# Optimization experiments

Measured on AMD Instinct MI355X. Metric: run time of the kernel, lower is better.

The kernel has to match this reference:

```python
import jax, jax.numpy as jnp
import numpy as np

N = 262144        # number of nodes
D = 64            # fixed in-degree per destination node (edges grouped by dest)
RATIO = 0.5
K = int(D * RATIO)  # edges kept per node = 32


def setup_inputs() -> dict:
    key = jax.random.key(0)
    k1, k2 = jax.random.split(key)
    logits = jax.random.normal(k1, (N,), dtype=jnp.float32)
    # source endpoints: random nodes; destination endpoints: sorted, D edges per node
    src = jax.random.randint(k2, (N * D,), 0, N, dtype=jnp.int32)
    dst = jnp.repeat(jnp.arange(N, dtype=jnp.int32), D)
    edge_index = jnp.stack([src, dst])  # [2, E]
    return {"logits": logits, "edge_index": edge_index}


def reference(logits, edge_index):
    # LabelAwarePool.forward: sigmoid -> per-edge L1 similarity -> per-dest-node top-k edges
    s = jax.nn.sigmoid(logits).reshape(-1)          # [N]
    ends = s[edge_index]                            # [2, E] endpoint scores
    sim = 1.0 - jnp.abs(ends[0] - ends[1])          # [E] similarity
    E = edge_index.shape[1]
    n = E // D                                      # number of segments (nodes)
    # segmented top-k: edges are grouped by destination node in blocks of D
    _, idx = jax.lax.top_k(sim.reshape(n, D), K)    # [n, K] indices within each segment
    edges_g = edge_index.reshape(2, n, D)           # [2, n, D]
    sel = jnp.take_along_axis(edges_g, idx[None, :, :], axis=2)  # [2, n, K]
    return sel.reshape(2, n * K)                    # concatenated kept edges
```

## Files before the change

kernel.cpp:

```cpp
#include <hip/hip_runtime.h>
#include <cstdint>

#define D_EDGES 64
#define K_KEEP  32

typedef unsigned long long ull;
typedef int v4i __attribute__((ext_vector_type(4)));

__device__ __forceinline__ float np_expf(float x) {
    const float log2e     = 1.44269504088896341f;
    const float cvt_magic = 12582912.0f;
    const float neg_ln2hi = -0.693359375f;
    const float neg_ln2lo = 2.12194440e-4f;
    const float p0 = 1.9875691500E-4f;
    const float p1 = 1.3981999507E-3f;
    const float p2 = 8.3334519073E-3f;
    const float p3 = 4.1665795894E-2f;
    const float p4 = 1.6666665459E-1f;
    const float p5 = 5.0000001201E-1f;

    float q = fmaf(x, log2e, cvt_magic);
    q -= cvt_magic;
    x = fmaf(q, neg_ln2hi, x);
    x = fmaf(q, neg_ln2lo, x);
    float x2 = x * x;
    float poly = fmaf(p0, x, p1);
    poly = fmaf(poly, x, p2);
    poly = fmaf(poly, x, p3);
    poly = fmaf(poly, x, p4);
    poly = fmaf(poly, x, p5);
    poly = fmaf(poly, x2, x);
    poly = poly + 1.0f;
    return ldexpf(poly, (int)q);
}

__device__ __forceinline__ float sigmoid_np(float x) {
    float e = np_expf(-x);
    return 1.0f / (1.0f + e);
}

__global__ void sigmoid_kernel(const float* __restrict__ logits,
                               float* __restrict__ s, int n) {
    int i = blockIdx.x * blockDim.x + threadIdx.x;
    if (i < n) s[i] = sigmoid_np(logits[i]);
}

__device__ __forceinline__ float gather_agent(const float* p) {
    return __hip_atomic_load(p, __ATOMIC_RELAXED, __HIP_MEMORY_SCOPE_AGENT);
}

template <int CTRL>
__device__ __forceinline__ ull xor_dpp_u64(ull v) {
    int lo = (int)(unsigned)v;
    int hi = (int)(v >> 32);
    lo = __builtin_amdgcn_update_dpp(lo, lo, CTRL, 0xF, 0xF, true);
    hi = __builtin_amdgcn_update_dpp(hi, hi, CTRL, 0xF, 0xF, true);
    return ((ull)(unsigned)hi << 32) | (unsigned)lo;
}

__device__ __forceinline__ ull xor4_swz_u64(ull v) {
    int lo = (int)(unsigned)v;
    int hi = (int)(v >> 32);
    lo = __builtin_amdgcn_ds_swizzle(lo, 0x101F);
    hi = __builtin_amdgcn_ds_swizzle(hi, 0x101F);
    return ((ull)(unsigned)hi << 32) | (unsigned)lo;
}

template <int DIST>
__device__ __forceinline__ ull lane_xor_u64(ull v) {
    if constexpr (DIST == 1)      return xor_dpp_u64<0xB1>(v);
    else if constexpr (DIST == 2) return xor_dpp_u64<0x4E>(v);
    else if constexpr (DIST == 4) return xor4_swz_u64(v);
    else                          return xor_dpp_u64<0x128>(v);
}

template <int K, int S1>
__device__ __forceinline__ void lce(ull& ka, ull& kb, int t) {
    bool up = (((4 * t + S1) & K) == 0);
    bool mf = ka > kb;
    if (mf != up) { ull tmp = ka; ka = kb; kb = tmp; }
}

template <int K, int J, int S>
__device__ __forceinline__ void cce(ull& k, int t) {
    ull other = lane_xor_u64<J / 4>(k);
    int e = 4 * t + S;
    bool up  = ((e & K) == 0);
    bool low = ((e & J) == 0);
    bool mf  = k > other;
    if (mf != (low == up)) k = other;
}

template <int K, int J>
__device__ __forceinline__ void cce4(ull& k0, ull& k1, ull& k2, ull& k3, int t) {
    cce<K, J, 0>(k0, t);
    cce<K, J, 1>(k1, t);
    cce<K, J, 2>(k2, t);
    cce<K, J, 3>(k3, t);
}

template <int K>
__device__ __forceinline__ void lceJ1(ull& k0, ull& k1, ull& k2, ull& k3, int t) {
    lce<K, 0>(k0, k1, t);
    lce<K, 2>(k2, k3, t);
}

template <int K>
__device__ __forceinline__ void lceJ2(ull& k0, ull& k1, ull& k2, ull& k3, int t) {
    lce<K, 0>(k0, k2, t);
    lce<K, 1>(k1, k3, t);
}

__device__ __forceinline__ ull make_key(float sim, int e, int src) {
    unsigned sb  = __float_as_uint(sim);
    unsigned e63 = (unsigned)(e ^ 63);
    unsigned hi  = (sb << 2) | (e63 >> 4);
    unsigned lo  = (e63 << 28) | (unsigned)src;
    return ((ull)hi << 32) | lo;
}

template <bool USE_TABLE>
__global__ void __launch_bounds__(256)
topk_kernel(const int* __restrict__ edge_index,
            const float* __restrict__ s,
            const float* __restrict__ logits,
            int* __restrict__ out,
            long long E, long long nseg) {
    long long gtid = (long long)blockIdx.x * blockDim.x + threadIdx.x;
    long long w = gtid >> 6;
    int lane = (int)(gtid & 63);
    int q = lane >> 4;
    int t = lane & 15;
    long long g = w * 4 + q;
    if (g >= nseg) return;

    v4i sv = __builtin_nontemporal_load(
        reinterpret_cast<const v4i*>(edge_index + g * D_EDGES + 4 * t));
    int dstv = edge_index[E + g * D_EDGES];

    float sd, ss0, ss1, ss2, ss3;
    if constexpr (USE_TABLE) {
        sd  = s[dstv];
        ss0 = gather_agent(s + sv.x);
        ss1 = gather_agent(s + sv.y);
        ss2 = gather_agent(s + sv.z);
        ss3 = gather_agent(s + sv.w);
    } else {
        sd  = sigmoid_np(logits[dstv]);
        ss0 = sigmoid_np(gather_agent(logits + sv.x));
        ss1 = sigmoid_np(gather_agent(logits + sv.y));
        ss2 = sigmoid_np(gather_agent(logits + sv.z));
        ss3 = sigmoid_np(gather_agent(logits + sv.w));
    }

    ull k0 = make_key(1.0f - fabsf(ss0 - sd), 4 * t + 0, sv.x);
    ull k1 = make_key(1.0f - fabsf(ss1 - sd), 4 * t + 1, sv.y);
    ull k2 = make_key(1.0f - fabsf(ss2 - sd), 4 * t + 2, sv.z);
    ull k3 = make_key(1.0f - fabsf(ss3 - sd), 4 * t + 3, sv.w);

    lceJ1<2>(k0, k1, k2, k3, t);
    lceJ2<4>(k0, k1, k2, k3, t);   lceJ1<4>(k0, k1, k2, k3, t);
    cce4<8, 4>(k0, k1, k2, k3, t);
    lceJ2<8>(k0, k1, k2, k3, t);   lceJ1<8>(k0, k1, k2, k3, t);
    cce4<16, 8>(k0, k1, k2, k3, t);
    cce4<16, 4>(k0, k1, k2, k3, t);
    lceJ2<16>(k0, k1, k2, k3, t);  lceJ1<16>(k0, k1, k2, k3, t);
    cce4<32, 16>(k0, k1, k2, k3, t);
    cce4<32, 8>(k0, k1, k2, k3, t);
    cce4<32, 4>(k0, k1, k2, k3, t);
    lceJ2<32>(k0, k1, k2, k3, t);  lceJ1<32>(k0, k1, k2, k3, t);
    cce4<64, 32>(k0, k1, k2, k3, t);
    cce4<64, 16>(k0, k1, k2, k3, t);
    cce4<64, 8>(k0, k1, k2, k3, t);
    cce4<64, 4>(k0, k1, k2, k3, t);
    lceJ2<64>(k0, k1, k2, k3, t);  lceJ1<64>(k0, k1, k2, k3, t);

    if (t < 8) {
        long long base = g * K_KEEP + 4 * t;
        v4i r0;
        r0.x = (int)(k0 & 0x0FFFFFFFu);
        r0.y = (int)(k1 & 0x0FFFFFFFu);
        r0.z = (int)(k2 & 0x0FFFFFFFu);
        r0.w = (int)(k3 & 0x0FFFFFFFu);
        v4i dv;
        dv.x = dstv; dv.y = dstv; dv.z = dstv; dv.w = dstv;
        __builtin_nontemporal_store(r0, reinterpret_cast<v4i*>(out + base));
        __builtin_nontemporal_store(dv, reinterpret_cast<v4i*>(out + nseg * K_KEEP + base));
    }
}

extern "C" void kernel_launch(void* const* d_in, const int* in_sizes, int n_in,
                              void* d_out, int out_size, void* d_ws, size_t ws_size,
                              hipStream_t stream) {
    const float* logits = (const float*)d_in[0];
    const int* edge_index = (const int*)d_in[1];
    int N = in_sizes[0];
    long long E = (long long)in_sizes[1] / 2;
    long long nseg = E / D_EDGES;
    int* out = (int*)d_out;

    long long nwave = (nseg + 3) / 4;
    long long total_threads = nwave * 64;
    int blocks = (int)((total_threads + 255) / 256);

    if (ws_size >= (size_t)N * sizeof(float)) {
        float* s = (float*)d_ws;
        sigmoid_kernel<<<(N + 255) / 256, 256, 0, stream>>>(logits, s, N);
        topk_kernel<true><<<blocks, 256, 0, stream>>>(edge_index, s, logits, out, E, nseg);
    } else {
        topk_kernel<false><<<blocks, 256, 0, stream>>>(edge_index, nullptr, logits, out, E, nseg);
    }
}
```

Before: 250.0 us.

## Sort 8 keys per lane with 8 lanes per segment in bitonic top-k

Each 64-edge segment is now handled by 8 lanes holding 8 keys each instead of 16 lanes holding 4. More bitonic compare-exchange stages run inside a lane's registers, so fewer cross-lane DPP/swizzle shuffles are needed, and each wave processes 8 segments. The launch uses half as many threads, at the cost of more registers per thread and less thread-level parallelism for hiding gather latency.

Result: slower. 258.3 us (+3.3%).

```diff
diff --git a/kernel.cpp b/kernel.cpp
--- a/kernel.cpp
+++ b/kernel.cpp
@@ -70,21 +70,21 @@
 __device__ __forceinline__ ull lane_xor_u64(ull v) {
     if constexpr (DIST == 1)      return xor_dpp_u64<0xB1>(v);
     else if constexpr (DIST == 2) return xor_dpp_u64<0x4E>(v);
-    else if constexpr (DIST == 4) return xor4_swz_u64(v);
-    else                          return xor_dpp_u64<0x128>(v);
-}
-
-template <int K, int S1>
-__device__ __forceinline__ void lce(ull& ka, ull& kb, int t) {
-    bool up = (((4 * t + S1) & K) == 0);
+    else                          return xor4_swz_u64(v);
+}
+
+
+template <int K, int E0>
+__device__ __forceinline__ void lce8(ull& ka, ull& kb, int t) {
+    bool up = (((8 * t + E0) & K) == 0);
     bool mf = ka > kb;
     if (mf != up) { ull tmp = ka; ka = kb; kb = tmp; }
 }
 
 template <int K, int J, int S>
-__device__ __forceinline__ void cce(ull& k, int t) {
-    ull other = lane_xor_u64<J / 4>(k);
-    int e = 4 * t + S;
+__device__ __forceinline__ void cce8(ull& k, int t) {
+    ull other = lane_xor_u64<J / 8>(k);
+    int e = 8 * t + S;
     bool up  = ((e & K) == 0);
     bool low = ((e & J) == 0);
     bool mf  = k > other;
@@ -92,23 +92,33 @@
 }
 
 template <int K, int J>
-__device__ __forceinline__ void cce4(ull& k0, ull& k1, ull& k2, ull& k3, int t) {
-    cce<K, J, 0>(k0, t);
-    cce<K, J, 1>(k1, t);
-    cce<K, J, 2>(k2, t);
-    cce<K, J, 3>(k3, t);
+__device__ __forceinline__ void cross8(ull& k0, ull& k1, ull& k2, ull& k3,
+                                       ull& k4, ull& k5, ull& k6, ull& k7, int t) {
+    cce8<K, J, 0>(k0, t); cce8<K, J, 1>(k1, t);
+    cce8<K, J, 2>(k2, t); cce8<K, J, 3>(k3, t);
+    cce8<K, J, 4>(k4, t); cce8<K, J, 5>(k5, t);
+    cce8<K, J, 6>(k6, t); cce8<K, J, 7>(k7, t);
 }
 
 template <int K>
-__device__ __forceinline__ void lceJ1(ull& k0, ull& k1, ull& k2, ull& k3, int t) {
-    lce<K, 0>(k0, k1, t);
-    lce<K, 2>(k2, k3, t);
+__device__ __forceinline__ void inlane1(ull& k0, ull& k1, ull& k2, ull& k3,
+                                        ull& k4, ull& k5, ull& k6, ull& k7, int t) {
+    lce8<K, 0>(k0, k1, t); lce8<K, 2>(k2, k3, t);
+    lce8<K, 4>(k4, k5, t); lce8<K, 6>(k6, k7, t);
 }
 
 template <int K>
-__device__ __forceinline__ void lceJ2(ull& k0, ull& k1, ull& k2, ull& k3, int t) {
-    lce<K, 0>(k0, k2, t);
-    lce<K, 1>(k1, k3, t);
+__device__ __forceinline__ void inlane2(ull& k0, ull& k1, ull& k2, ull& k3,
+                                        ull& k4, ull& k5, ull& k6, ull& k7, int t) {
+    lce8<K, 0>(k0, k2, t); lce8<K, 1>(k1, k3, t);
+    lce8<K, 4>(k4, k6, t); lce8<K, 5>(k5, k7, t);
+}
+
+template <int K>
+__device__ __forceinline__ void inlane4(ull& k0, ull& k1, ull& k2, ull& k3,
+                                        ull& k4, ull& k5, ull& k6, ull& k7, int t) {
+    lce8<K, 0>(k0, k4, t); lce8<K, 1>(k1, k5, t);
+    lce8<K, 2>(k2, k6, t); lce8<K, 3>(k3, k7, t);
 }
 
 __device__ __forceinline__ ull make_key(float sim, int e, int src) {
@@ -129,63 +139,75 @@
     long long gtid = (long long)blockIdx.x * blockDim.x + threadIdx.x;
     long long w = gtid >> 6;
     int lane = (int)(gtid & 63);
-    int q = lane >> 4;
-    int t = lane & 15;
-    long long g = w * 4 + q;
+    int q = lane >> 3;
+    int t = lane & 7;
+    long long g = w * 8 + q;
     if (g >= nseg) return;
 
-    v4i sv = __builtin_nontemporal_load(
-        reinterpret_cast<const v4i*>(edge_index + g * D_EDGES + 4 * t));
+    const int* ebase = edge_index + g * D_EDGES + 8 * t;
+    v4i sva = __builtin_nontemporal_load(reinterpret_cast<const v4i*>(ebase));
+    v4i svb = __builtin_nontemporal_load(reinterpret_cast<const v4i*>(ebase + 4));
     int dstv = edge_index[E + g * D_EDGES];
 
-    float sd, ss0, ss1, ss2, ss3;
+    float sd, ss0, ss1, ss2, ss3, ss4, ss5, ss6, ss7;
     if constexpr (USE_TABLE) {
         sd  = s[dstv];
-        ss0 = gather_agent(s + sv.x);
-        ss1 = gather_agent(s + sv.y);
-        ss2 = gather_agent(s + sv.z);
-        ss3 = gather_agent(s + sv.w);
+        ss0 = gather_agent(s + sva.x); ss1 = gather_agent(s + sva.y);
+        ss2 = gather_agent(s + sva.z); ss3 = gather_agent(s + sva.w);
+        ss4 = gather_agent(s + svb.x); ss5 = gather_agent(s + svb.y);
+        ss6 = gather_agent(s + svb.z); ss7 = gather_agent(s + svb.w);
     } else {
         sd  = sigmoid_np(logits[dstv]);
-        ss0 = sigmoid_np(gather_agent(logits + sv.x));
-        ss1 = sigmoid_np(gather_agent(logits + sv.y));
-        ss2 = sigmoid_np(gather_agent(logits + sv.z));
-        ss3 = sigmoid_np(gather_agent(logits + sv.w));
+        ss0 = sigmoid_np(gather_agent(logits + sva.x));
+        ss1 = sigmoid_np(gather_agent(logits + sva.y));
+        ss2 = sigmoid_np(gather_agent(logits + sva.z));
+        ss3 = sigmoid_np(gather_agent(logits + sva.w));
+        ss4 = sigmoid_np(gather_agent(logits + svb.x));
+        ss5 = sigmoid_np(gather_agent(logits + svb.y));
+        ss6 = sigmoid_np(gather_agent(logits + svb.z));
+        ss7 = sigmoid_np(gather_agent(logits + svb.w));
     }
 
-    ull k0 = make_key(1.0f - fabsf(ss0 - sd), 4 * t + 0, sv.x);
-    ull k1 = make_key(1.0f - fabsf(ss1 - sd), 4 * t + 1, sv.y);
-    ull k2 = make_key(1.0f - fabsf(ss2 - sd), 4 * t + 2, sv.z);
-    ull k3 = make_key(1.0f - fabsf(ss3 - sd), 4 * t + 3, sv.w);
-
-    lceJ1<2>(k0, k1, k2, k3, t);
-    lceJ2<4>(k0, k1, k2, k3, t);   lceJ1<4>(k0, k1, k2, k3, t);
-    cce4<8, 4>(k0, k1, k2, k3, t);
-    lceJ2<8>(k0, k1, k2, k3, t);   lceJ1<8>(k0, k1, k2, k3, t);
-    cce4<16, 8>(k0, k1, k2, k3, t);
-    cce4<16, 4>(k0, k1, k2, k3, t);
-    lceJ2<16>(k0, k1, k2, k3, t);  lceJ1<16>(k0, k1, k2, k3, t);
-    cce4<32, 16>(k0, k1, k2, k3, t);
-    cce4<32, 8>(k0, k1, k2, k3, t);
-    cce4<32, 4>(k0, k1, k2, k3, t);
-    lceJ2<32>(k0, k1, k2, k3, t);  lceJ1<32>(k0, k1, k2, k3, t);
-    cce4<64, 32>(k0, k1, k2, k3, t);
-    cce4<64, 16>(k0, k1, k2, k3, t);
-    cce4<64, 8>(k0, k1, k2, k3, t);
-    cce4<64, 4>(k0, k1, k2, k3, t);
-    lceJ2<64>(k0, k1, k2, k3, t);  lceJ1<64>(k0, k1, k2, k3, t);
-
-    if (t < 8) {
-        long long base = g * K_KEEP + 4 * t;
-        v4i r0;
-        r0.x = (int)(k0 & 0x0FFFFFFFu);
-        r0.y = (int)(k1 & 0x0FFFFFFFu);
-        r0.z = (int)(k2 & 0x0FFFFFFFu);
-        r0.w = (int)(k3 & 0x0FFFFFFFu);
-        v4i dv;
+    ull k0 = make_key(1.0f - fabsf(ss0 - sd), 8 * t + 0, sva.x);
+    ull k1 = make_key(1.0f - fabsf(ss1 - sd), 8 * t + 1, sva.y);
+    ull k2 = make_key(1.0f - fabsf(ss2 - sd), 8 * t + 2, sva.z);
+    ull k3 = make_key(1.0f - fabsf(ss3 - sd), 8 * t + 3, sva.w);
+    ull k4 = make_key(1.0f - fabsf(ss4 - sd), 8 * t + 4, svb.x);
+    ull k5 = make_key(1.0f - fabsf(ss5 - sd), 8 * t + 5, svb.y);
+    ull k6 = make_key(1.0f - fabsf(ss6 - sd), 8 * t + 6, svb.z);
+    ull k7 = make_key(1.0f - fabsf(ss7 - sd), 8 * t + 7, svb.w);
+
+    inlane1<2>(k0,k1,k2,k3,k4,k5,k6,k7,t);
+    inlane2<4>(k0,k1,k2,k3,k4,k5,k6,k7,t);   inlane1<4>(k0,k1,k2,k3,k4,k5,k6,k7,t);
+    inlane4<8>(k0,k1,k2,k3,k4,k5,k6,k7,t);
+    inlane2<8>(k0,k1,k2,k3,k4,k5,k6,k7,t);   inlane1<8>(k0,k1,k2,k3,k4,k5,k6,k7,t);
+    cross8<16, 8>(k0,k1,k2,k3,k4,k5,k6,k7,t);
+    inlane4<16>(k0,k1,k2,k3,k4,k5,k6,k7,t);
+    inlane2<16>(k0,k1,k2,k3,k4,k5,k6,k7,t);  inlane1<16>(k0,k1,k2,k3,k4,k5,k6,k7,t);
+    cross8<32, 16>(k0,k1,k2,k3,k4,k5,k6,k7,t);
+    cross8<32, 8>(k0,k1,k2,k3,k4,k5,k6,k7,t);
+    inlane4<32>(k0,k1,k2,k3,k4,k5,k6,k7,t);
+    inlane2<32>(k0,k1,k2,k3,k4,k5,k6,k7,t);  inlane1<32>(k0,k1,k2,k3,k4,k5,k6,k7,t);
+    cross8<64, 32>(k0,k1,k2,k3,k4,k5,k6,k7,t);
+    cross8<64, 16>(k0,k1,k2,k3,k4,k5,k6,k7,t);
+    cross8<64, 8>(k0,k1,k2,k3,k4,k5,k6,k7,t);
+    inlane4<64>(k0,k1,k2,k3,k4,k5,k6,k7,t);
+    inlane2<64>(k0,k1,k2,k3,k4,k5,k6,k7,t);  inlane1<64>(k0,k1,k2,k3,k4,k5,k6,k7,t);
+
+    if (t < 4) {
+        long long base = g * K_KEEP + 8 * t;
+        v4i ra, rb, dv;
+        ra.x = (int)(k0 & 0x0FFFFFFFu); ra.y = (int)(k1 & 0x0FFFFFFFu);
+        ra.z = (int)(k2 & 0x0FFFFFFFu); ra.w = (int)(k3 & 0x0FFFFFFFu);
+        rb.x = (int)(k4 & 0x0FFFFFFFu); rb.y = (int)(k5 & 0x0FFFFFFFu);
+        rb.z = (int)(k6 & 0x0FFFFFFFu); rb.w = (int)(k7 & 0x0FFFFFFFu);
         dv.x = dstv; dv.y = dstv; dv.z = dstv; dv.w = dstv;
-        __builtin_nontemporal_store(r0, reinterpret_cast<v4i*>(out + base));
-        __builtin_nontemporal_store(dv, reinterpret_cast<v4i*>(out + nseg * K_KEEP + base));
+        int* o0 = out + base;
+        int* o1 = out + nseg * K_KEEP + base;
+        __builtin_nontemporal_store(ra, reinterpret_cast<v4i*>(o0));
+        __builtin_nontemporal_store(rb, reinterpret_cast<v4i*>(o0 + 4));
+        __builtin_nontemporal_store(dv, reinterpret_cast<v4i*>(o1));
+        __builtin_nontemporal_store(dv, reinterpret_cast<v4i*>(o1 + 4));
     }
 }
 
@@ -199,7 +221,7 @@
     long long nseg = E / D_EDGES;
     int* out = (int*)d_out;
 
-    long long nwave = (nseg + 3) / 4;
+    long long nwave = (nseg + 7) / 8;
     long long total_threads = nwave * 64;
     int blocks = (int)((total_threads + 255) / 256);
 
```
